# Kernel optimization log

Hardware: AMD Instinct MI355X
Metric: run time of the kernel (lower is better)

Reference implementation:

```python
import jax, jax.numpy as jnp
import numpy as np

BATCH, SEQ_LEN, HIDDEN, N_TYPES = 8, 1024, 256, 4
MAX_SPAN = 12


def _span_indices(seq_len: int, max_span_length: int):
    # Enumerate (start, end) pairs in the exact order of the original triple loop:
    # start ascending, end ascending within [start, min(start+max_span, seq_len)).
    starts, ends = [], []
    for s in range(seq_len):
        for e in range(s, min(s + max_span_length, seq_len)):
            starts.append(s)
            ends.append(e)
    return np.asarray(starts, np.int32), np.asarray(ends, np.int32)


def setup_inputs() -> dict:
    key = jax.random.key(0)
    k1, k2, k3 = jax.random.split(key, 3)
    hidden_states = jax.random.normal(k1, (BATCH, SEQ_LEN, HIDDEN), dtype=jnp.float32)
    # Stacked nn.Linear(2H -> H) weights for each entity type: W[t] has shape [H, 2H]
    W = jax.random.normal(k2, (N_TYPES, HIDDEN, 2 * HIDDEN), dtype=jnp.float32) * 0.02
    b = jax.random.normal(k3, (N_TYPES, HIDDEN), dtype=jnp.float32) * 0.02
    return {"hidden_states": hidden_states, "W": W, "b": b, "max_span_length": MAX_SPAN}


def reference(hidden_states, W, b, max_span_length):
    B, S, H = hidden_states.shape
    T = W.shape[0]
    start_idx, end_idx = _span_indices(S, int(max_span_length))  # [N]
    N = start_idx.shape[0]
    h_start = hidden_states[:, start_idx, :]          # [B, N, H]
    h_end = hidden_states[:, end_idx, :]              # [B, N, H]
    cat = jnp.concatenate([h_start, h_end], axis=-1)  # [B, N, 2H]
    # Per-type linear: y = x @ W_t^T + b_t, entity type is the innermost stacking axis
    out = jnp.einsum('bnc,thc->bnth', cat, W) + b     # [B, N, T, H]
    return out.reshape(B, N * T, H)
```

## Files before the change

kernel.cpp:

```cpp
#include <hip/hip_runtime.h>
#include <hip/hip_bf16.h>
#include <cstdint>
#include <cstddef>

#define BATCH   8
#define SEQLEN  1024
#define HIDDEN  256
#define NTYPES  4
#define NSPAN   12222
#define NFULL   12156
#define NPAD    12288
#define KDIM    512
#define NCOL    1024
#define MROWS   8192
#define PCOLS   2048

typedef __bf16 bf16x8 __attribute__((ext_vector_type(8)));
typedef float  f32x4  __attribute__((ext_vector_type(4)));
struct alignas(8) B4 { __bf16 a, b, c, d; };

#define AS1 __attribute__((address_space(1)))
#define AS3 __attribute__((address_space(3)))

__device__ __forceinline__ void load16(const __bf16* g, __bf16* l) {
    __builtin_amdgcn_global_load_lds((AS1 const void*)g, (AS3 void*)l, 16, 0, 0);
}

__device__ __forceinline__ f32x4 cvt4(B4 v) {
    return (f32x4){(float)v.a, (float)v.b, (float)v.c, (float)v.d};
}

__global__ void cvt_bf16(const float* __restrict__ src, __bf16* __restrict__ dst, int n) {
    int i = (blockIdx.x * 256 + threadIdx.x) * 4;
    if (i + 3 < n) {
        float4 f = *(const float4*)(src + i);
        B4 v;
        v.a = (__bf16)f.x; v.b = (__bf16)f.y; v.c = (__bf16)f.z; v.d = (__bf16)f.w;
        *(B4*)(dst + i) = v;
    }
}

__global__ void mk_wbf2(const float* __restrict__ W, __bf16* __restrict__ dst) {
    int idx = (blockIdx.x * 256 + threadIdx.x) * 4;
    int jp = idx >> 8, k = idx & 255;
    int t = (jp & 1023) >> 8, h = jp & 255;
    int c = k + ((jp >> 10) << 8);
    float4 f = *(const float4*)(W + ((size_t)(t * 256 + h)) * 512 + c);
    B4 v;
    v.a = (__bf16)f.x; v.b = (__bf16)f.y; v.c = (__bf16)f.z; v.d = (__bf16)f.w;
    *(B4*)(dst + idx) = v;
}

__global__ __launch_bounds__(256) void pgemm(
    const __bf16* __restrict__ A,
    const __bf16* __restrict__ Wbf2,
    __bf16*       __restrict__ P)
{
    __shared__ alignas(16) __bf16 As[128 * 32];
    __shared__ alignas(16) __bf16 Bs[128 * 32];

    const int tid  = threadIdx.x;
    const int wave = tid >> 6;
    const int lane = tid & 63;
    const int wm   = (wave >> 1) * 64;
    const int wn   = (wave & 1) * 64;
    const int lr   = lane & 15;
    const int lq   = lane >> 4;

    const int j0 = blockIdx.x * 128;
    const int m0 = blockIdx.y * 128;

    const int l0  = wave * 1024 + lane * 8;
    const int l1  = l0 + 512;
    const int mm0 = l0 >> 5, kk0 = l0 & 31;
    const int mm1 = l1 >> 5, kk1 = l1 & 31;

    const __bf16* a0 = A     + (size_t)(m0 + mm0) * HIDDEN + kk0;
    const __bf16* a1 = A     + (size_t)(m0 + mm1) * HIDDEN + kk1;
    const __bf16* w0 = Wbf2 + (size_t)(j0 + mm0) * HIDDEN + kk0;
    const __bf16* w1 = Wbf2 + (size_t)(j0 + mm1) * HIDDEN + kk1;

    f32x4 acc[4][4];
#pragma unroll
    for (int i = 0; i < 4; ++i)
#pragma unroll
        for (int j = 0; j < 4; ++j)
            acc[i][j] = (f32x4){0.f, 0.f, 0.f, 0.f};

    for (int ks = 0; ks < 8; ++ks) {
        const int c0 = ks * 32;
        __syncthreads();
        load16(a0 + c0, &As[l0]);
        load16(a1 + c0, &As[l1]);
        load16(w0 + c0, &Bs[l0]);
        load16(w1 + c0, &Bs[l1]);
        __syncthreads();

        bf16x8 af[4], bfv[4];
#pragma unroll
        for (int mi = 0; mi < 4; ++mi)
            af[mi] = *(const bf16x8*)(As + (wm + mi * 16 + lr) * 32 + lq * 8);
#pragma unroll
        for (int ni = 0; ni < 4; ++ni)
            bfv[ni] = *(const bf16x8*)(Bs + (wn + ni * 16 + lr) * 32 + lq * 8);
#pragma unroll
        for (int mi = 0; mi < 4; ++mi)
#pragma unroll
            for (int ni = 0; ni < 4; ++ni)
                acc[mi][ni] = __builtin_amdgcn_mfma_f32_16x16x32_bf16(
                    af[mi], bfv[ni], acc[mi][ni], 0, 0, 0);
    }

#pragma unroll
    for (int mi = 0; mi < 4; ++mi) {
#pragma unroll
        for (int r = 0; r < 4; ++r) {
            const int m = m0 + wm + mi * 16 + lq * 4 + r;
            __bf16* op = P + (size_t)m * PCOLS + (j0 + wn + lr);
#pragma unroll
            for (int ni = 0; ni < 4; ++ni)
                op[ni * 16] = (__bf16)acc[mi][ni][r];
        }
    }
}

__global__ __launch_bounds__(256) void span_epi(
    const __bf16* __restrict__ P,
    const float*  __restrict__ bias,
    float*        __restrict__ out,
    int b0)
{
    const int bx  = blockIdx.x;
    const int xcd = bx & 7;
    const int i   = bx >> 3;
    const int b   = b0 + (i >> 7);
    const int s   = xcd * 128 + (i & 127);
    const int j   = threadIdx.x * 4;

    const size_t prow = (size_t)((b - b0) * SEQLEN + s) * PCOLS;

    const f32x4 bv = *(const f32x4*)(bias + j);
    f32x4 ps = cvt4(*(const B4*)(P + prow + j)) + bv;

    int len; long nbase;
    if (s <= SEQLEN - 12) { len = 12; nbase = (long)s * 12; }
    else { len = SEQLEN - s; nbase = NFULL + (long)(1036 - s) * (s - 1013) / 2; }

    const __bf16* pe = P + prow + NCOL + j;
    B4 per[12];
#pragma unroll
    for (int k = 0; k < 12; ++k) {
        const int kk = k < len ? k : len - 1;
        per[k] = *(const B4*)(pe + (size_t)kk * PCOLS);
    }

    float* ob = out + ((size_t)b * NSPAN + nbase) * NCOL + j;
#pragma unroll
    for (int k = 0; k < 12; ++k) {
        if (k < len) {
            f32x4 o = ps + cvt4(per[k]);
            *(f32x4*)(ob + (size_t)k * NCOL) = o;
        }
    }
}

__global__ void mk_idx(int* __restrict__ sA, int* __restrict__ eA) {
    int n = blockIdx.x * 256 + threadIdx.x;
    if (n >= NPAD) return;
    int s = 0, e = 0;
    if (n < NFULL) {
        s = n / 12;
        e = s + (n - s * 12);
    } else if (n < NSPAN) {
        int r = n - NFULL;
        s = SEQLEN - 11;
        int cnt = 11;
        while (r >= cnt) { r -= cnt; --cnt; ++s; }
        e = s + r;
    }
    sA[n] = s; eA[n] = e;
}

__global__ __launch_bounds__(256) void span_gemm(
    const __bf16* __restrict__ Hbf,
    const __bf16* __restrict__ Wbf,
    const int*    __restrict__ idxS,
    const int*    __restrict__ idxE,
    const float*  __restrict__ bias,
    float*        __restrict__ out)
{
    __shared__ alignas(16) __bf16 As[128 * 32];
    __shared__ alignas(16) __bf16 Bs[128 * 32];

    const int tid  = threadIdx.x;
    const int wave = tid >> 6;
    const int lane = tid & 63;
    const int wm   = (wave >> 1) * 64;
    const int wn   = (wave & 1) * 64;
    const int lr   = lane & 15;
    const int lq   = lane >> 4;

    const int j0 = blockIdx.x * 128;
    const int n0 = blockIdx.y * 128;
    const int b  = blockIdx.z;

    const int l0  = wave * 1024 + lane * 8;
    const int l1  = l0 + 512;
    const int mm0 = l0 >> 5, kk0 = l0 & 31;
    const int mm1 = l1 >> 5, kk1 = l1 & 31;

    const int s0 = idxS[n0 + mm0], e0 = idxE[n0 + mm0];
    const int s1 = idxS[n0 + mm1], e1 = idxE[n0 + mm1];

    const __bf16* hb = Hbf + (size_t)b * (SEQLEN * HIDDEN);
    const __bf16* w0 = Wbf + (size_t)(j0 + mm0) * KDIM + kk0;
    const __bf16* w1 = Wbf + (size_t)(j0 + mm1) * KDIM + kk1;

    f32x4 acc[4][4];
#pragma unroll
    for (int i = 0; i < 4; ++i)
#pragma unroll
        for (int j = 0; j < 4; ++j)
            acc[i][j] = (f32x4){0.f, 0.f, 0.f, 0.f};

    for (int half = 0; half < 2; ++half) {
        const __bf16* a0  = hb + (half ? e0 : s0) * HIDDEN + kk0;
        const __bf16* a1  = hb + (half ? e1 : s1) * HIDDEN + kk1;
        const __bf16* wb0 = w0 + half * HIDDEN;
        const __bf16* wb1 = w1 + half * HIDDEN;

        for (int ks = 0; ks < 8; ++ks) {
            const int c0 = ks * 32;
            __syncthreads();
            load16(a0  + c0, &As[l0]);
            load16(a1  + c0, &As[l1]);
            load16(wb0 + c0, &Bs[l0]);
            load16(wb1 + c0, &Bs[l1]);
            __syncthreads();

            bf16x8 af[4], bfv[4];
#pragma unroll
            for (int mi = 0; mi < 4; ++mi)
                af[mi] = *(const bf16x8*)(As + (wm + mi * 16 + lr) * 32 + lq * 8);
#pragma unroll
            for (int ni = 0; ni < 4; ++ni)
                bfv[ni] = *(const bf16x8*)(Bs + (wn + ni * 16 + lr) * 32 + lq * 8);
#pragma unroll
            for (int mi = 0; mi < 4; ++mi)
#pragma unroll
                for (int ni = 0; ni < 4; ++ni)
                    acc[mi][ni] = __builtin_amdgcn_mfma_f32_16x16x32_bf16(
                        af[mi], bfv[ni], acc[mi][ni], 0, 0, 0);
        }
    }

    float bv[4];
#pragma unroll
    for (int ni = 0; ni < 4; ++ni) bv[ni] = bias[j0 + wn + ni * 16 + lr];

    const size_t obase = (size_t)b * NSPAN * NCOL;
#pragma unroll
    for (int mi = 0; mi < 4; ++mi) {
#pragma unroll
        for (int r = 0; r < 4; ++r) {
            const int n = n0 + wm + mi * 16 + lq * 4 + r;
            if (n < NSPAN) {
                float* op = out + obase + (size_t)n * NCOL + (j0 + wn + lr);
#pragma unroll
                for (int ni = 0; ni < 4; ++ni)
                    op[ni * 16] = acc[mi][ni][r] + bv[ni];
            }
        }
    }
}

extern "C" void kernel_launch(void* const* d_in, const int* in_sizes, int n_in,
                              void* d_out, int out_size, void* d_ws, size_t ws_size,
                              hipStream_t stream) {
    const float* hid  = (const float*)d_in[0];
    const float* W    = (const float*)d_in[1];
    const float* bias = (const float*)d_in[2];
    float* out = (float*)d_out;

    char* ws = (char*)d_ws;
    __bf16* Wb  = (__bf16*)ws;
    __bf16* Hbf = (__bf16*)(ws + (size_t)1048576);
    const size_t base      = (size_t)1048576 + 4194304;
    const size_t needFull  = base + (size_t)MROWS  * PCOLS * 2;
    const size_t needChunk = base + (size_t)SEQLEN * PCOLS * 2;

    cvt_bf16<<<2048, 256, 0, stream>>>(hid, Hbf, MROWS * HIDDEN);

    if (ws_size >= needFull) {
        __bf16* P = (__bf16*)(ws + base);
        mk_wbf2<<<512, 256, 0, stream>>>(W, Wb);
        pgemm<<<dim3(PCOLS / 128, MROWS / 128), 256, 0, stream>>>(Hbf, Wb, P);
        span_epi<<<BATCH * SEQLEN, 256, 0, stream>>>(P, bias, out, 0);
    } else if (ws_size >= needChunk) {
        __bf16* P = (__bf16*)(ws + base);
        mk_wbf2<<<512, 256, 0, stream>>>(W, Wb);
        for (int b = 0; b < BATCH; ++b) {
            pgemm<<<dim3(PCOLS / 128, SEQLEN / 128), 256, 0, stream>>>(
                Hbf + (size_t)b * SEQLEN * HIDDEN, Wb, P);
            span_epi<<<SEQLEN, 256, 0, stream>>>(P, bias, out, b);
        }
    } else {
        int* idxS = (int*)(ws + base);
        int* idxE = idxS + NPAD;
        cvt_bf16<<<512, 256, 0, stream>>>(W, Wb, NCOL * KDIM);
        mk_idx<<<NPAD / 256, 256, 0, stream>>>(idxS, idxE);
        span_gemm<<<dim3(8, 96, BATCH), 256, 0, stream>>>(Hbf, Wb, idxS, idxE, bias, out);
    }
}
```

Baseline: 436.7 us.

## Chunk batches for cache-resident P, fold bias into GEMM, use nontemporal output stores

The launch logic now processes the batch in chunks of up to 4 (or 2 or 1), sized to the workspace, instead of one full 8-batch pass. This keeps the bf16 intermediate P small enough to stay cache-resident between the GEMM and the span epilogue. The start-half bias is added in the pgemm epilogue before bf16 rounding, so span_epi no longer loads bias. The large fp32 output writes use nontemporal stores so they do not evict P from cache. The cost is extra kernel launches, and bias now passes through bf16 rounding.

```diff
diff --git a/kernel.cpp b/kernel.cpp
--- a/kernel.cpp
+++ b/kernel.cpp
@@ -54,6 +54,7 @@
 __global__ __launch_bounds__(256) void pgemm(
     const __bf16* __restrict__ A,
     const __bf16* __restrict__ Wbf2,
+    const float*  __restrict__ bias,
     __bf16*       __restrict__ P)
 {
     __shared__ alignas(16) __bf16 As[128 * 32];
@@ -75,8 +76,8 @@
     const int mm0 = l0 >> 5, kk0 = l0 & 31;
     const int mm1 = l1 >> 5, kk1 = l1 & 31;
 
-    const __bf16* a0 = A     + (size_t)(m0 + mm0) * HIDDEN + kk0;
-    const __bf16* a1 = A     + (size_t)(m0 + mm1) * HIDDEN + kk1;
+    const __bf16* a0 = A    + (size_t)(m0 + mm0) * HIDDEN + kk0;
+    const __bf16* a1 = A    + (size_t)(m0 + mm1) * HIDDEN + kk1;
     const __bf16* w0 = Wbf2 + (size_t)(j0 + mm0) * HIDDEN + kk0;
     const __bf16* w1 = Wbf2 + (size_t)(j0 + mm1) * HIDDEN + kk1;
 
@@ -111,6 +112,12 @@
                     af[mi], bfv[ni], acc[mi][ni], 0, 0, 0);
     }
 
+    float bv[4] = {0.f, 0.f, 0.f, 0.f};
+    if (j0 < NCOL) {
+#pragma unroll
+        for (int ni = 0; ni < 4; ++ni) bv[ni] = bias[j0 + wn + ni * 16 + lr];
+    }
+
 #pragma unroll
     for (int mi = 0; mi < 4; ++mi) {
 #pragma unroll
@@ -119,28 +126,26 @@
             __bf16* op = P + (size_t)m * PCOLS + (j0 + wn + lr);
 #pragma unroll
             for (int ni = 0; ni < 4; ++ni)
-                op[ni * 16] = (__bf16)acc[mi][ni][r];
+                op[ni * 16] = (__bf16)(acc[mi][ni][r] + bv[ni]);
         }
     }
 }
 
 __global__ __launch_bounds__(256) void span_epi(
     const __bf16* __restrict__ P,
-    const float*  __restrict__ bias,
     float*        __restrict__ out,
     int b0)
 {
-    const int bx  = blockIdx.x;
-    const int xcd = bx & 7;
-    const int i   = bx >> 3;
-    const int b   = b0 + (i >> 7);
-    const int s   = xcd * 128 + (i & 127);
-    const int j   = threadIdx.x * 4;
-
-    const size_t prow = (size_t)((b - b0) * SEQLEN + s) * PCOLS;
-
-    const f32x4 bv = *(const f32x4*)(bias + j);
-    f32x4 ps = cvt4(*(const B4*)(P + prow + j)) + bv;
+    const int bx   = blockIdx.x;
+    const int xcd  = bx & 7;
+    const int i    = bx >> 3;
+    const int brel = i >> 7;
+    const int b    = b0 + brel;
+    const int s    = xcd * 128 + (i & 127);
+    const int j    = threadIdx.x * 4;
+
+    const size_t prow = (size_t)(brel * SEQLEN + s) * PCOLS;
+    const f32x4 ps = cvt4(*(const B4*)(P + prow + j));
 
     int len; long nbase;
     if (s <= SEQLEN - 12) { len = 12; nbase = (long)s * 12; }
@@ -159,7 +164,7 @@
     for (int k = 0; k < 12; ++k) {
         if (k < len) {
             f32x4 o = ps + cvt4(per[k]);
-            *(f32x4*)(ob + (size_t)k * NCOL) = o;
+            __builtin_nontemporal_store(o, (f32x4*)(ob + (size_t)k * NCOL));
         }
     }
 }
@@ -285,24 +290,23 @@
     char* ws = (char*)d_ws;
     __bf16* Wb  = (__bf16*)ws;
     __bf16* Hbf = (__bf16*)(ws + (size_t)1048576);
-    const size_t base      = (size_t)1048576 + 4194304;
-    const size_t needFull  = base + (size_t)MROWS  * PCOLS * 2;
-    const size_t needChunk = base + (size_t)SEQLEN * PCOLS * 2;
+    const size_t base  = (size_t)1048576 + 4194304;
+    const size_t CHUNK = (size_t)SEQLEN * PCOLS * 2;
+
+    int nb = 0;
+    if      (ws_size >= base + 4 * CHUNK) nb = 4;
+    else if (ws_size >= base + 2 * CHUNK) nb = 2;
+    else if (ws_size >= base + 1 * CHUNK) nb = 1;
 
     cvt_bf16<<<2048, 256, 0, stream>>>(hid, Hbf, MROWS * HIDDEN);
 
-    if (ws_size >= needFull) {
+    if (nb) {
         __bf16* P = (__bf16*)(ws + base);
         mk_wbf2<<<512, 256, 0, stream>>>(W, Wb);
-        pgemm<<<dim3(PCOLS / 128, MROWS / 128), 256, 0, stream>>>(Hbf, Wb, P);
-        span_epi<<<BATCH * SEQLEN, 256, 0, stream>>>(P, bias, out, 0);
-    } else if (ws_size >= needChunk) {
-        __bf16* P = (__bf16*)(ws + base);
-        mk_wbf2<<<512, 256, 0, stream>>>(W, Wb);
-        for (int b = 0; b < BATCH; ++b) {
-            pgemm<<<dim3(PCOLS / 128, SEQLEN / 128), 256, 0, stream>>>(
-                Hbf + (size_t)b * SEQLEN * HIDDEN, Wb, P);
-            span_epi<<<SEQLEN, 256, 0, stream>>>(P, bias, out, b);
+        for (int b0 = 0; b0 < BATCH; b0 += nb) {
+            pgemm<<<dim3(PCOLS / 128, nb * SEQLEN / 128), 256, 0, stream>>>(
+                Hbf + (size_t)b0 * SEQLEN * HIDDEN, Wb, bias, P);
+            span_epi<<<nb * SEQLEN, 256, 0, stream>>>(P, out, b0);
         }
     } else {
         int* idxS = (int*)(ws + base);
```

Measured after the change: 435.0 us. About the same (-0.4%).
